# Optimization experiments

Hardware: AMD Instinct MI355X
Metric: run time of the kernel (lower is better)

The kernel has to match this reference:

```python
import jax, jax.numpy as jnp
import numpy as np

T, B, H, V, L = 512, 8, 256, 32000, 3
THRESH = 1.0

# Heaviside spike with ATan surrogate gradient (snntorch default, alpha=2)
@jax.custom_vjp
def spike(u):
    return (u > 0).astype(u.dtype)

def _spike_fwd(u):
    return (u > 0).astype(u.dtype), u

def _spike_bwd(u, g):
    return (g / (1.0 + (jnp.pi * u) ** 2),)

spike.defvjp(_spike_fwd, _spike_bwd)


def leaky_scan(cur, beta):
    """mem[t] = beta * mem[t-1] + cur[t]; cur: (T,B,H), beta: (H,). No reset -> associative."""
    def step(mem, c):
        mem = beta * mem + c
        return mem, mem
    _, mems = jax.lax.scan(step, jnp.zeros(cur.shape[1:], cur.dtype), cur)
    return mems  # (T,B,H)


def setup_inputs() -> dict:
    key = jax.random.key(0)
    ks = jax.random.split(key, 10)
    s = 1.0 / np.sqrt(H)
    return {
        "tokens": jax.random.randint(ks[0], (T, B), 0, V),
        "token_emb": jax.random.normal(ks[1], (V, H), dtype=jnp.float32) * 0.02,
        "pos_emb": jax.random.normal(ks[2], (T, H), dtype=jnp.float32) * 0.02,
        "Wq": jax.random.normal(ks[3], (L, H, H), dtype=jnp.float32) * s,
        "bq": jnp.zeros((L, H), dtype=jnp.float32),
        "beta": jax.random.uniform(ks[4], (L, H), minval=0.5, maxval=0.95),
        "Wfc": jax.random.normal(ks[5], (L, H, H), dtype=jnp.float32) * s,
        "bfc": jnp.zeros((L, H), dtype=jnp.float32),
        "Wout": jax.random.normal(ks[6], (H, V), dtype=jnp.float32) * s,
        "bout": jnp.zeros((V,), dtype=jnp.float32),
    }


def reference(tokens, token_emb, pos_emb, Wq, bq, beta, Wfc, bfc, Wout, bout):
    # embed: (T,B,H) + broadcast positional (T,1,H)
    h = token_emb[tokens] + pos_emb[:, None, :]
    for l in range(L):  # small fixed layer count
        cur = jnp.einsum('tbh,hd->tbd', h, Wq[l]) + bq[l]   # q-projection
        mem = leaky_scan(cur, beta[l])                       # leaky integrate, no reset
        spk = spike(mem - THRESH)                            # heaviside spikes
        h = jax.nn.relu(jnp.einsum('tbh,hd->tbd', spk, Wfc[l]) + bfc[l])
    logits = jnp.einsum('tbh,hv->tbv', h, Wout) + bout       # (T,B,V)
    return logits
```

## Files before the change

kernel.cpp:

```cpp
#include <hip/hip_runtime.h>
#include <hip/hip_bf16.h>
#include <cstddef>

constexpr int T_ = 512;
constexpr int B_ = 8;
constexpr int H_ = 256;
constexpr int V_ = 32000;
constexpr int L_ = 3;
constexpr int M_ = T_ * B_;

typedef __attribute__((ext_vector_type(8))) short short8;
typedef __attribute__((ext_vector_type(4))) float floatx4;

__device__ __forceinline__ unsigned short f2bf(float f) {
    unsigned u = __float_as_uint(f);
    u += 0x7fffu + ((u >> 16) & 1u);
    return (unsigned short)(u >> 16);
}

__device__ __forceinline__ void gl_lds16(const void* g, void* l) {
    __builtin_amdgcn_global_load_lds((__attribute__((address_space(1))) void*)g,
                                     (__attribute__((address_space(3))) void*)l,
                                     16, 0, 0);
}

__global__ __launch_bounds__(256) void embed_kernel(
    const int* __restrict__ tokens, const float* __restrict__ temb,
    const float* __restrict__ pemb, unsigned short* __restrict__ hb)
{
    const int idx = blockIdx.x * 256 + threadIdx.x;
    const int h4 = idx & (H_ / 4 - 1);
    const int tb = idx >> 6;
    const int b  = tb & (B_ - 1);
    const int t  = tb >> 3;
    const int tok = tokens[t * B_ + b];
    const float4 e = *(const float4*)&temb[(size_t)tok * H_ + h4 * 4];
    const float4 p = *(const float4*)&pemb[(size_t)t * H_ + h4 * 4];
    ushort4 r;
    r.x = f2bf(e.x + p.x); r.y = f2bf(e.y + p.y);
    r.z = f2bf(e.z + p.z); r.w = f2bf(e.w + p.w);
    *(ushort4*)&hb[(size_t)idx * 4] = r;
}

constexpr int CH_ = 32;
constexpr int NT_ = T_ / CH_;
constexpr int TS_ = B_ * H_;

__global__ __launch_bounds__(256) void scan_local_kernel(
    const float* __restrict__ cur, const float* __restrict__ beta_l,
    float* __restrict__ mloc)
{
    const int c = blockIdx.x, b = blockIdx.y, h = threadIdx.x;
    const float bt = beta_l[h];
    const size_t off = ((size_t)(c * CH_) * B_ + b) * H_ + h;
    const float* p = cur + off;
    float* q = mloc + off;
    float mem = 0.0f;
    #pragma unroll
    for (int tt = 0; tt < CH_; ++tt) {
        mem = fmaf(bt, mem, p[(size_t)tt * TS_]);
        q[(size_t)tt * TS_] = mem;
    }
}

__global__ __launch_bounds__(256) void scan_apply_kernel(
    const float* __restrict__ mloc, const float* __restrict__ beta_l,
    unsigned short* __restrict__ spk)
{
    const int c = blockIdx.x, b = blockIdx.y, h = threadIdx.x;
    const float bt = beta_l[h];
    float b32 = bt;
    #pragma unroll
    for (int i = 0; i < 5; ++i) b32 *= b32;
    float carry = 0.0f;
    for (int j = 0; j < c; ++j)
        carry = fmaf(b32, carry,
                     mloc[((size_t)(j * CH_ + CH_ - 1) * B_ + b) * H_ + h]);
    const size_t off = ((size_t)(c * CH_) * B_ + b) * H_ + h;
    const float* p = mloc + off;
    unsigned short* q = spk + off;
    float pw = bt;
    #pragma unroll
    for (int tt = 0; tt < CH_; ++tt) {
        const float mem = fmaf(pw, carry, p[(size_t)tt * TS_]);
        pw *= bt;
        q[(size_t)tt * TS_] = (mem > 1.0f) ? (unsigned short)0x3F80u
                                           : (unsigned short)0u;
    }
}

__global__ __launch_bounds__(256) void transpose_small_kernel(
    const float* __restrict__ Wq, const float* __restrict__ Wfc,
    unsigned short* __restrict__ WT)
{
    __shared__ float t[64][65];
    const int z = blockIdx.z;
    const float* src = (z < 3) ? Wq + (size_t)z * H_ * H_
                               : Wfc + (size_t)(z - 3) * H_ * H_;
    unsigned short* dst = WT + (size_t)z * H_ * H_;
    const int n0 = blockIdx.x * 64, k0 = blockIdx.y * 64;
    const int x = threadIdx.x & 63, y = threadIdx.x >> 6;
    #pragma unroll
    for (int i = 0; i < 16; ++i)
        t[y + 4 * i][x] = src[(size_t)(k0 + y + 4 * i) * H_ + n0 + x];
    __syncthreads();
    #pragma unroll
    for (int i = 0; i < 16; ++i)
        dst[(size_t)(n0 + y + 4 * i) * H_ + k0 + x] = f2bf(t[x][y + 4 * i]);
}

__global__ __launch_bounds__(256) void transpose_wout_kernel(
    const float* __restrict__ W, unsigned short* __restrict__ Wt)
{
    __shared__ float t[64][65];
    const int n0 = blockIdx.x * 64;
    const int k0 = blockIdx.y * 64;
    const int x = threadIdx.x & 63, y = threadIdx.x >> 6;
    #pragma unroll
    for (int i = 0; i < 16; ++i)
        t[y + 4 * i][x] = W[(size_t)(k0 + y + 4 * i) * V_ + n0 + x];
    __syncthreads();
    #pragma unroll
    for (int i = 0; i < 16; ++i)
        Wt[(size_t)(n0 + y + 4 * i) * H_ + k0 + x] = f2bf(t[x][y + 4 * i]);
}


__global__ __launch_bounds__(256, 2) void gemm_mfma_out(
    const unsigned short* __restrict__ A,
    const unsigned short* __restrict__ Bt,
    const float* __restrict__ bias,
    float* __restrict__ C)
{
    constexpr int K = H_, N = V_;
    __shared__ __align__(16) short lA[2048][8];
    __shared__ __align__(16) short lB[1024][8];

    const int tid = threadIdx.x;
    const int lane = tid & 63, wave = tid >> 6;
    const int wm = wave >> 1, wn = wave & 1;
    const int l15 = lane & 15, quad = lane >> 4;
    const int m0 = blockIdx.x * 256;
    const int n0 = blockIdx.y * 128;

    floatx4 acc[8][4] = {};

    for (int k0 = 0; k0 < K; k0 += 64) {
        #pragma unroll
        for (int j = 0; j < 8; ++j) {
            const int base = (wave * 8 + j) * 64;
            const int s = base + lane;
            const int row = s >> 3;
            const int oct = (s & 7) ^ (row & 7);
            gl_lds16(A + (size_t)(m0 + row) * K + k0 + oct * 8, &lA[base][0]);
        }
        #pragma unroll
        for (int j = 0; j < 4; ++j) {
            const int base = (wave * 4 + j) * 64;
            const int s = base + lane;
            const int row = s >> 3;
            const int oct = (s & 7) ^ (row & 7);
            gl_lds16(Bt + (size_t)(n0 + row) * K + k0 + oct * 8, &lB[base][0]);
        }
        __syncthreads();

        #pragma unroll
        for (int t = 0; t < 2; ++t) {
            short8 af[8], bf[4];
            #pragma unroll
            for (int f = 0; f < 8; ++f) {
                const int ra = wm * 128 + f * 16 + l15;
                af[f] = *(const short8*)&lA[ra * 8 + ((4 * t + quad) ^ (ra & 7))][0];
            }
            #pragma unroll
            for (int g = 0; g < 4; ++g) {
                const int rb = wn * 64 + g * 16 + l15;
                bf[g] = *(const short8*)&lB[rb * 8 + ((4 * t + quad) ^ (rb & 7))][0];
            }
            #pragma unroll
            for (int f = 0; f < 8; ++f)
                #pragma unroll
                for (int g = 0; g < 4; ++g)
                    acc[f][g] = __builtin_amdgcn_mfma_f32_16x16x32_bf16(
                        af[f], bf[g], acc[f][g], 0, 0, 0);
        }
        __syncthreads();
    }

    float* scr = (float*)&lA[0][0] + (size_t)wave * 1088;
    float bvv[4];
    #pragma unroll
    for (int g = 0; g < 4; ++g)
        bvv[g] = bias[n0 + wn * 64 + g * 16 + l15];

    #pragma unroll
    for (int f = 0; f < 8; ++f) {
        #pragma unroll
        for (int g = 0; g < 4; ++g)
            #pragma unroll
            for (int r = 0; r < 4; ++r)
                scr[(quad * 4 + r) * 68 + g * 16 + l15] = acc[f][g][r] + bvv[g];
        __syncthreads();
        #pragma unroll
        for (int rr = 0; rr < 4; ++rr) {
            const int ml = rr * 4 + quad;
            const floatx4 v = *(const floatx4*)&scr[ml * 68 + l15 * 4];
            const size_t m = (size_t)(m0 + wm * 128 + f * 16 + ml);
            __builtin_nontemporal_store(
                v, (floatx4*)&C[m * (size_t)N + n0 + wn * 64 + l15 * 4]);
        }
        __syncthreads();
    }
}

template <int RELU, int OUT_BF16>
__global__ __launch_bounds__(256) void gemm_mfma_layer(
    const unsigned short* __restrict__ A,
    const unsigned short* __restrict__ Bt,
    const float* __restrict__ bias,
    float* __restrict__ Cf, unsigned short* __restrict__ Cb)
{
    constexpr int K = H_, N = H_;
    __shared__ __align__(16) short lA[1024][8];
    __shared__ __align__(16) short lB[512][8];

    const int tid = threadIdx.x;
    const int lane = tid & 63, wave = tid >> 6;
    const int wm = wave >> 1, wn = wave & 1;
    const int l15 = lane & 15, quad = lane >> 4;
    const int m0 = blockIdx.x * 128;
    const int n0 = blockIdx.y * 64;

    floatx4 acc[4][2] = {};

    for (int k0 = 0; k0 < K; k0 += 64) {
        #pragma unroll
        for (int j = 0; j < 4; ++j) {
            const int base = (wave * 4 + j) * 64;
            const int s = base + lane;
            const int row = s >> 3;
            const int oct = (s & 7) ^ (row & 7);
            gl_lds16(A + (size_t)(m0 + row) * K + k0 + oct * 8, &lA[base][0]);
        }
        #pragma unroll
        for (int j = 0; j < 2; ++j) {
            const int base = (wave * 2 + j) * 64;
            const int s = base + lane;
            const int row = s >> 3;
            const int oct = (s & 7) ^ (row & 7);
            gl_lds16(Bt + (size_t)(n0 + row) * K + k0 + oct * 8, &lB[base][0]);
        }
        __syncthreads();

        #pragma unroll
        for (int t = 0; t < 2; ++t) {
            short8 af[4], bf[2];
            #pragma unroll
            for (int f = 0; f < 4; ++f) {
                const int ra = wm * 64 + f * 16 + l15;
                af[f] = *(const short8*)&lA[ra * 8 + ((4 * t + quad) ^ (ra & 7))][0];
            }
            #pragma unroll
            for (int f = 0; f < 2; ++f) {
                const int rb = wn * 32 + f * 16 + l15;
                bf[f] = *(const short8*)&lB[rb * 8 + ((4 * t + quad) ^ (rb & 7))][0];
            }
            #pragma unroll
            for (int i = 0; i < 4; ++i)
                #pragma unroll
                for (int j2 = 0; j2 < 2; ++j2)
                    acc[i][j2] = __builtin_amdgcn_mfma_f32_16x16x32_bf16(
                        af[i], bf[j2], acc[i][j2], 0, 0, 0);
        }
        __syncthreads();
    }

    #pragma unroll
    for (int j2 = 0; j2 < 2; ++j2) {
        const int col = n0 + wn * 32 + j2 * 16 + l15;
        const float bv = bias[col];
        #pragma unroll
        for (int i = 0; i < 4; ++i) {
            const int rbase = m0 + wm * 64 + i * 16 + quad * 4;
            #pragma unroll
            for (int r = 0; r < 4; ++r) {
                float v = acc[i][j2][r] + bv;
                if (RELU) v = fmaxf(v, 0.0f);
                if (OUT_BF16)
                    Cb[(size_t)(rbase + r) * N + col] = f2bf(v);
                else
                    Cf[(size_t)(rbase + r) * N + col] = v;
            }
        }
    }
}

extern "C" void kernel_launch(void* const* d_in, const int* in_sizes, int n_in,
                              void* d_out, int out_size, void* d_ws, size_t ws_size,
                              hipStream_t stream)
{
    const int*   tokens = (const int*)  d_in[0];
    const float* temb   = (const float*)d_in[1];
    const float* pemb   = (const float*)d_in[2];
    const float* Wq     = (const float*)d_in[3];
    const float* bq     = (const float*)d_in[4];
    const float* beta   = (const float*)d_in[5];
    const float* Wfc    = (const float*)d_in[6];
    const float* bfc    = (const float*)d_in[7];
    const float* Wout   = (const float*)d_in[8];
    const float* bout   = (const float*)d_in[9];
    float* out = (float*)d_out;

    unsigned short* h_bf  = (unsigned short*)d_ws;
    unsigned short* spk   = h_bf + (size_t)M_ * H_;
    unsigned short* WT    = spk + (size_t)M_ * H_;
    unsigned short* WoutT = WT + (size_t)2 * L_ * H_ * H_;
    float*          cur   = (float*)(WoutT + (size_t)V_ * H_);
    float*          mloc  = cur + (size_t)M_ * H_;

    transpose_small_kernel<<<dim3(4, 4, 6), 256, 0, stream>>>(Wq, Wfc, WT);
    transpose_wout_kernel<<<dim3(V_ / 64, H_ / 64), 256, 0, stream>>>(Wout, WoutT);

    embed_kernel<<<(M_ * H_ / 4) / 256, 256, 0, stream>>>(tokens, temb, pemb, h_bf);

    for (int l = 0; l < L_; ++l) {
        const unsigned short* WqT  = WT + (size_t)l * H_ * H_;
        const unsigned short* WfcT = WT + (size_t)(L_ + l) * H_ * H_;
        gemm_mfma_layer<0, 0><<<dim3(M_ / 128, H_ / 64), 256, 0, stream>>>(
            h_bf, WqT, bq + (size_t)l * H_, cur, nullptr);
        scan_local_kernel<<<dim3(NT_, B_), 256, 0, stream>>>(
            cur, beta + (size_t)l * H_, mloc);
        scan_apply_kernel<<<dim3(NT_, B_), 256, 0, stream>>>(
            mloc, beta + (size_t)l * H_, spk);
        gemm_mfma_layer<1, 1><<<dim3(M_ / 128, H_ / 64), 256, 0, stream>>>(
            spk, WfcT, bfc + (size_t)l * H_, nullptr, h_bf);
    }

    gemm_mfma_out<<<dim3(M_ / 256, V_ / 128), 256, 0, stream>>>(
        h_bf, WoutT, bout, out);
}
```

Before: 657.2 us.

## Restructure output GEMM into small M tiles with full-K B in LDS and swizzled grid

The vocab-projection GEMM now uses 64x128 tiles instead of 256x128. The whole K=256 slice of Wout for the tile is loaded into LDS once, and A is double-buffered across K steps. A 1D grid with a custom block-to-tile mapping groups blocks that share N columns, aiming to keep Wout tiles in L2 and improve load balance across CUs. Accumulators shrink, which may raise occupancy, but per-block LDS (64KB+16KB) is large and each block recomputes less, so more A traffic is re-read.

Result: slower. 703.5 us (+7.0%).

```diff
diff --git a/kernel.cpp b/kernel.cpp
--- a/kernel.cpp
+++ b/kernel.cpp
@@ -125,7 +125,6 @@
         Wt[(size_t)(n0 + y + 4 * i) * H_ + k0 + x] = f2bf(t[x][y + 4 * i]);
 }
 
-
 __global__ __launch_bounds__(256, 2) void gemm_mfma_out(
     const unsigned short* __restrict__ A,
     const unsigned short* __restrict__ Bt,
@@ -133,52 +132,73 @@
     float* __restrict__ C)
 {
     constexpr int K = H_, N = V_;
-    __shared__ __align__(16) short lA[2048][8];
-    __shared__ __align__(16) short lB[1024][8];
+    __shared__ __align__(16) short lB[4096][8];
+    __shared__ __align__(16) short lA[2][512][8];
 
     const int tid = threadIdx.x;
     const int lane = tid & 63, wave = tid >> 6;
     const int wm = wave >> 1, wn = wave & 1;
     const int l15 = lane & 15, quad = lane >> 4;
-    const int m0 = blockIdx.x * 256;
-    const int n0 = blockIdx.y * 128;
-
-    floatx4 acc[8][4] = {};
-
-    for (int k0 = 0; k0 < K; k0 += 64) {
-        #pragma unroll
-        for (int j = 0; j < 8; ++j) {
-            const int base = (wave * 8 + j) * 64;
-            const int s = base + lane;
-            const int row = s >> 3;
-            const int oct = (s & 7) ^ (row & 7);
-            gl_lds16(A + (size_t)(m0 + row) * K + k0 + oct * 8, &lA[base][0]);
-        }
-        #pragma unroll
-        for (int j = 0; j < 4; ++j) {
-            const int base = (wave * 4 + j) * 64;
-            const int s = base + lane;
-            const int row = s >> 3;
-            const int oct = (s & 7) ^ (row & 7);
-            gl_lds16(Bt + (size_t)(n0 + row) * K + k0 + oct * 8, &lB[base][0]);
-        }
-        __syncthreads();
-
+
+    const int id = blockIdx.x;
+    int cls, local;
+    if (id < 4096) { cls = id >> 11;        local = id & 2047; }
+    else           { cls = 2 + (id - 4096) / 1984; local = (id - 4096) % 1984; }
+    const int s  = (local >> 6) * 8 + cls;
+    const int mb = local & 63;
+    const int m0 = mb * 64, n0 = s * 128;
+
+    #pragma unroll
+    for (int g = 0; g < 16; ++g) {
+        const int bse = (wave * 16 + g) * 64;
+        const int sl = bse + lane;
+        const int row = sl >> 5;
+        const int oct = (sl & 24) | ((sl & 7) ^ (row & 7));
+        gl_lds16(Bt + (size_t)(n0 + row) * K + oct * 8, &lB[bse][0]);
+    }
+    #pragma unroll
+    for (int g = 0; g < 2; ++g) {
+        const int bse = (wave * 2 + g) * 64;
+        const int sl = bse + lane;
+        const int row = sl >> 3;
+        const int oct = (sl & 7) ^ (row & 7);
+        gl_lds16(A + (size_t)(m0 + row) * K + oct * 8, &lA[0][bse][0]);
+    }
+    __syncthreads();
+
+    floatx4 acc[2][4] = {};
+
+    #pragma unroll
+    for (int k0 = 0; k0 < 4; ++k0) {
+        if (k0 < 3) {
+            #pragma unroll
+            for (int g = 0; g < 2; ++g) {
+                const int bse = (wave * 2 + g) * 64;
+                const int sl = bse + lane;
+                const int row = sl >> 3;
+                const int oct = (sl & 7) ^ (row & 7);
+                gl_lds16(A + (size_t)(m0 + row) * K + (k0 + 1) * 64 + oct * 8,
+                         &lA[(k0 + 1) & 1][bse][0]);
+            }
+        }
         #pragma unroll
         for (int t = 0; t < 2; ++t) {
-            short8 af[8], bf[4];
-            #pragma unroll
-            for (int f = 0; f < 8; ++f) {
-                const int ra = wm * 128 + f * 16 + l15;
-                af[f] = *(const short8*)&lA[ra * 8 + ((4 * t + quad) ^ (ra & 7))][0];
+            short8 af[2], bf[4];
+            #pragma unroll
+            for (int f = 0; f < 2; ++f) {
+                const int ra = wm * 32 + f * 16 + l15;
+                af[f] = *(const short8*)
+                    &lA[k0 & 1][ra * 8 + ((t * 4 + quad) ^ (ra & 7))][0];
             }
             #pragma unroll
             for (int g = 0; g < 4; ++g) {
                 const int rb = wn * 64 + g * 16 + l15;
-                bf[g] = *(const short8*)&lB[rb * 8 + ((4 * t + quad) ^ (rb & 7))][0];
-            }
-            #pragma unroll
-            for (int f = 0; f < 8; ++f)
+                const int o = k0 * 8 + t * 4 + quad;
+                const int os = (o & 24) | ((o & 7) ^ (rb & 7));
+                bf[g] = *(const short8*)&lB[rb * 32 + os][0];
+            }
+            #pragma unroll
+            for (int f = 0; f < 2; ++f)
                 #pragma unroll
                 for (int g = 0; g < 4; ++g)
                     acc[f][g] = __builtin_amdgcn_mfma_f32_16x16x32_bf16(
@@ -187,29 +207,27 @@
         __syncthreads();
     }
 
-    float* scr = (float*)&lA[0][0] + (size_t)wave * 1088;
+    float* scr = (float*)&lB[0][0] + wave * (32 * 68);
     float bvv[4];
     #pragma unroll
     for (int g = 0; g < 4; ++g)
         bvv[g] = bias[n0 + wn * 64 + g * 16 + l15];
-
-    #pragma unroll
-    for (int f = 0; f < 8; ++f) {
+    #pragma unroll
+    for (int f = 0; f < 2; ++f)
         #pragma unroll
         for (int g = 0; g < 4; ++g)
             #pragma unroll
             for (int r = 0; r < 4; ++r)
-                scr[(quad * 4 + r) * 68 + g * 16 + l15] = acc[f][g][r] + bvv[g];
-        __syncthreads();
-        #pragma unroll
-        for (int rr = 0; rr < 4; ++rr) {
-            const int ml = rr * 4 + quad;
-            const floatx4 v = *(const floatx4*)&scr[ml * 68 + l15 * 4];
-            const size_t m = (size_t)(m0 + wm * 128 + f * 16 + ml);
-            __builtin_nontemporal_store(
-                v, (floatx4*)&C[m * (size_t)N + n0 + wn * 64 + l15 * 4]);
-        }
-        __syncthreads();
+                scr[(f * 16 + quad * 4 + r) * 68 + g * 16 + l15] =
+                    acc[f][g][r] + bvv[g];
+    __syncthreads();
+    #pragma unroll
+    for (int j = 0; j < 8; ++j) {
+        const int ml = j * 4 + quad;
+        const floatx4 v = *(const floatx4*)&scr[ml * 68 + l15 * 4];
+        const size_t m = (size_t)(m0 + wm * 32 + ml);
+        __builtin_nontemporal_store(
+            v, (floatx4*)&C[m * (size_t)N + n0 + wn * 64 + l15 * 4]);
     }
 }
 
@@ -336,6 +354,6 @@
             spk, WfcT, bfc + (size_t)l * H_, nullptr, h_bf);
     }
 
-    gemm_mfma_out<<<dim3(M_ / 256, V_ / 128), 256, 0, stream>>>(
+    gemm_mfma_out<<<(M_ / 64) * (V_ / 128), 256, 0, stream>>>(
         h_bf, WoutT, bout, out);
 }
```

## Double-buffer output GEMM LDS tiles with K=32 stages and drop epilogue barriers

Applied to the files above, without the earlier changes.

The vocab-projection GEMM now uses two LDS buffers with K-steps of 32, so the async global-to-LDS loads for the next step are issued before the MFMA work on the current one, replacing a single-buffer K=64 load-then-compute loop. The swizzle changes to four 16-byte chunks per row. The epilogue block-wide barriers are removed because each wave only touches its own scratch region. The cost is one barrier per K-step (8 instead of 4), and since the global_load_lds writes are asynchronous, correctness relies on barrier and wait semantics covering the in-flight buffer.

Measured after the change: 666.4 us. Within noise of the previous version (+1.4%).

```diff
diff --git a/kernel.cpp b/kernel.cpp
--- a/kernel.cpp
+++ b/kernel.cpp
@@ -125,7 +125,6 @@
         Wt[(size_t)(n0 + y + 4 * i) * H_ + k0 + x] = f2bf(t[x][y + 4 * i]);
 }
 
-
 __global__ __launch_bounds__(256, 2) void gemm_mfma_out(
     const unsigned short* __restrict__ A,
     const unsigned short* __restrict__ Bt,
@@ -133,8 +132,8 @@
     float* __restrict__ C)
 {
     constexpr int K = H_, N = V_;
-    __shared__ __align__(16) short lA[2048][8];
-    __shared__ __align__(16) short lB[1024][8];
+    __shared__ __align__(16) short lA[2][1024][8];
+    __shared__ __align__(16) short lB[2][512][8];
 
     const int tid = threadIdx.x;
     const int lane = tid & 63, wave = tid >> 6;
@@ -145,49 +144,55 @@
 
     floatx4 acc[8][4] = {};
 
-    for (int k0 = 0; k0 < K; k0 += 64) {
-        #pragma unroll
-        for (int j = 0; j < 8; ++j) {
-            const int base = (wave * 8 + j) * 64;
-            const int s = base + lane;
-            const int row = s >> 3;
-            const int oct = (s & 7) ^ (row & 7);
-            gl_lds16(A + (size_t)(m0 + row) * K + k0 + oct * 8, &lA[base][0]);
-        }
-        #pragma unroll
-        for (int j = 0; j < 4; ++j) {
-            const int base = (wave * 4 + j) * 64;
-            const int s = base + lane;
-            const int row = s >> 3;
-            const int oct = (s & 7) ^ (row & 7);
-            gl_lds16(Bt + (size_t)(n0 + row) * K + k0 + oct * 8, &lB[base][0]);
-        }
+    auto stage = [&](int kk, int buf) {
+        #pragma unroll
+        for (int g = 0; g < 4; ++g) {
+            const int base = (wave * 4 + g) * 64;
+            const int sl = base + lane;
+            const int row = sl >> 2;
+            const int oct = (sl & 3) ^ (row & 3);
+            gl_lds16(A + (size_t)(m0 + row) * K + kk * 32 + oct * 8,
+                     &lA[buf][base][0]);
+        }
+        #pragma unroll
+        for (int g = 0; g < 2; ++g) {
+            const int base = (wave * 2 + g) * 64;
+            const int sl = base + lane;
+            const int row = sl >> 2;
+            const int oct = (sl & 3) ^ (row & 3);
+            gl_lds16(Bt + (size_t)(n0 + row) * K + kk * 32 + oct * 8,
+                     &lB[buf][base][0]);
+        }
+    };
+
+    stage(0, 0);
+    __syncthreads();
+
+    #pragma unroll
+    for (int kk = 0; kk < 8; ++kk) {
+        if (kk < 7) stage(kk + 1, (kk + 1) & 1);
+
+        short8 af[8], bf[4];
+        #pragma unroll
+        for (int f = 0; f < 8; ++f) {
+            const int ra = wm * 128 + f * 16 + l15;
+            af[f] = *(const short8*)&lA[kk & 1][ra * 4 + (quad ^ (ra & 3))][0];
+        }
+        #pragma unroll
+        for (int g = 0; g < 4; ++g) {
+            const int rb = wn * 64 + g * 16 + l15;
+            bf[g] = *(const short8*)&lB[kk & 1][rb * 4 + (quad ^ (rb & 3))][0];
+        }
+        #pragma unroll
+        for (int f = 0; f < 8; ++f)
+            #pragma unroll
+            for (int g = 0; g < 4; ++g)
+                acc[f][g] = __builtin_amdgcn_mfma_f32_16x16x32_bf16(
+                    af[f], bf[g], acc[f][g], 0, 0, 0);
         __syncthreads();
-
-        #pragma unroll
-        for (int t = 0; t < 2; ++t) {
-            short8 af[8], bf[4];
-            #pragma unroll
-            for (int f = 0; f < 8; ++f) {
-                const int ra = wm * 128 + f * 16 + l15;
-                af[f] = *(const short8*)&lA[ra * 8 + ((4 * t + quad) ^ (ra & 7))][0];
-            }
-            #pragma unroll
-            for (int g = 0; g < 4; ++g) {
-                const int rb = wn * 64 + g * 16 + l15;
-                bf[g] = *(const short8*)&lB[rb * 8 + ((4 * t + quad) ^ (rb & 7))][0];
-            }
-            #pragma unroll
-            for (int f = 0; f < 8; ++f)
-                #pragma unroll
-                for (int g = 0; g < 4; ++g)
-                    acc[f][g] = __builtin_amdgcn_mfma_f32_16x16x32_bf16(
-                        af[f], bf[g], acc[f][g], 0, 0, 0);
-        }
-        __syncthreads();
-    }
-
-    float* scr = (float*)&lA[0][0] + (size_t)wave * 1088;
+    }
+
+    float* scr = (float*)&lA[0][0][0] + (size_t)wave * 1088;
     float bvv[4];
     #pragma unroll
     for (int g = 0; g < 4; ++g)
@@ -200,7 +205,6 @@
             #pragma unroll
             for (int r = 0; r < 4; ++r)
                 scr[(quad * 4 + r) * 68 + g * 16 + l15] = acc[f][g][r] + bvv[g];
-        __syncthreads();
         #pragma unroll
         for (int rr = 0; rr < 4; ++rr) {
             const int ml = rr * 4 + quad;
@@ -209,7 +213,6 @@
             __builtin_nontemporal_store(
                 v, (floatx4*)&C[m * (size_t)N + n0 + wn * 64 + l15 * 4]);
         }
-        __syncthreads();
     }
 }
 
```
